# Performance work log

Hardware: AMD Instinct MI355X
Metric: run time of the kernel (lower is better)

The kernel has to match this reference:

```python
import jax, jax.numpy as jnp
import numpy as np

DEGREE = 8
D = 512
K = 256
O = 512
N = 65536


def setup_inputs() -> dict:
    key = jax.random.key(0)
    ks = jax.random.split(key, 4)
    z = jax.random.normal(ks[0], (N, D), dtype=jnp.float32)
    T0 = jnp.ones((K,), dtype=jnp.float32)
    # T[i-1] corresponds to parameter T_i, i = 1..DEGREE, each [K, D]
    T = jax.random.normal(ks[1], (DEGREE, K, D), dtype=jnp.float32) * 0.02
    C_w = jax.random.normal(ks[2], (O, K), dtype=jnp.float32) * (1.0 / np.sqrt(K))
    C_b = jnp.zeros((O,), dtype=jnp.float32)
    return {"z": z, "T0": T0, "T": T, "C_w": C_w, "C_b": C_b}


def reference(z, T0, T, C_w, C_b):
    # z: [N, D]; T: [DEGREE, K, D]; recurrence over polynomial degree n:
    #   out_n = (z @ ((2n-1)/n * T_n).T) * out_{n-1} - (n-1)/n * out_{n-2}
    z = z.reshape(-1, D)
    out_prev2 = T0                                  # degree 0, [K] (broadcasts over N)
    out_prev1 = jnp.einsum('nd,kd->nk', z, T[0])    # degree 1, [N, K]
    for n in range(2, DEGREE + 1):
        a = (2.0 * n - 1.0) / n
        b = (n - 1.0) / n
        cur = jnp.einsum('nd,kd->nk', z, a * T[n - 1]) * out_prev1 - b * out_prev2
        out_prev2, out_prev1 = out_prev1, cur
    # layer_C applied to out_list[degree]
    return out_prev1 @ C_w.T + C_b
```

## Files before the change

kernel.cpp:

```cpp
#include <hip/hip_runtime.h>
#include <hip/hip_fp16.h>
#include <cstdint>

#define NROWS 65536
#define DIM   512
#define KDIM  256
#define ODIM  512
#define DEG   8
#define ZN    (NROWS * DIM)
#define TN    (DEG * KDIM * DIM)
#define CWN   (ODIM * KDIM)

typedef _Float16 f16x8 __attribute__((ext_vector_type(8)));
typedef float    f32x4 __attribute__((ext_vector_type(4)));


__device__ __forceinline__ void gld_lds16(const void* g, void* l) {
  __builtin_amdgcn_global_load_lds(
      (const __attribute__((address_space(1))) unsigned int*)g,
      (__attribute__((address_space(3))) unsigned int*)l, 16, 0, 0);
}

__device__ __forceinline__ unsigned pack2h(float a, float b) {
  union { _Float16 h[2]; unsigned u; } x;
  x.h[0] = (_Float16)a; x.h[1] = (_Float16)b;
  return x.u;
}

__device__ __forceinline__ int swz(int row, int chunk) {
  return (row << 7) | (((chunk + row) & 7) << 4);
}


__global__ void k_convert(const float* __restrict__ z,
                          const float* __restrict__ T,
                          const float* __restrict__ Cw,
                          _Float16* __restrict__ z16,
                          _Float16* __restrict__ Tb,
                          _Float16* __restrict__ Cwb) {
  long e = ((long)blockIdx.x * 256 + threadIdx.x) * 4;
  const float* src;
  _Float16* dst;
  float s = 1.0f;
  if (e < ZN) {
    src = z + e; dst = z16 + e;
  } else {
    long o = e - ZN;
    if (o < TN) {
      int n = (int)(o >> 17);
      s = (n == 0) ? 1.0f : (float)(2 * n + 1) / (float)(n + 1);
      src = T + o; dst = Tb + o;
    } else {
      long c = o - TN;
      if (c >= CWN) return;
      src = Cw + c; dst = Cwb + c;
    }
  }
  float4 v = *(const float4*)src;
  uint2 p; p.x = pack2h(v.x * s, v.y * s); p.y = pack2h(v.z * s, v.w * s);
  *(uint2*)dst = p;
}


__launch_bounds__(256, 3)
__global__ void k_poly(const _Float16* __restrict__ z16,
                       const float* __restrict__ T0,
                       const _Float16* __restrict__ Tb,
                       _Float16* __restrict__ u8) {
  __shared__ __align__(16) uint16_t As[128 * 64];
  __shared__ __align__(16) uint16_t Bs[128 * 64];

  const int tid = threadIdx.x;
  const int wave = tid >> 6, lane = tid & 63;

  const int id = blockIdx.x;
  const int super = id >> 8, rem = id & 255;
  const int kg = rem >> 4;
  const int rt = (super << 4) | (rem & 15);
  const int r0 = rt << 7;
  const int k0 = kg << 4;

  const int m_l = lane & 15, kq = lane >> 4;
  const int wrow = wave << 5;

  f32x4 acc[DEG][2];
#pragma unroll
  for (int n = 0; n < DEG; n++)
#pragma unroll
    for (int a = 0; a < 2; a++)
      acc[n][a] = (f32x4){0.f, 0.f, 0.f, 0.f};

  const _Float16* aptr[4];
  const _Float16* bptr[4];
  int lofs[4];
#pragma unroll
  for (int j = 0; j < 4; j++) {
    int lin = (j << 8) + tid;
    int row = lin >> 3;
    int c = ((lin & 7) - row) & 7;
    lofs[j] = lin << 4;
    aptr[j] = z16 + (size_t)(r0 + row) * DIM + (c << 3);
    int n = row >> 4, kk = row & 15;
    bptr[j] = Tb + (size_t)((n << 8) + k0 + kk) * DIM + (c << 3);
  }

  for (int it = 0; it < DIM / 64; it++) {
    __syncthreads();
#pragma unroll
    for (int j = 0; j < 4; j++) gld_lds16(aptr[j], (char*)As + lofs[j]);
#pragma unroll
    for (int j = 0; j < 4; j++) gld_lds16(bptr[j], (char*)Bs + lofs[j]);
#pragma unroll
    for (int j = 0; j < 4; j++) { aptr[j] += 64; bptr[j] += 64; }
    __syncthreads();

#pragma unroll
    for (int ks = 0; ks < 2; ks++) {
      const int chunk = (ks << 2) + kq;
      f16x8 af[2];
#pragma unroll
      for (int mf = 0; mf < 2; mf++)
        af[mf] = *(const f16x8*)((char*)As + swz(wrow + (mf << 4) + m_l, chunk));
#pragma unroll
      for (int n = 0; n < DEG; n++) {
        f16x8 bv = *(const f16x8*)((char*)Bs + swz((n << 4) + m_l, chunk));
#pragma unroll
        for (int mf = 0; mf < 2; mf++)
          acc[n][mf] = __builtin_amdgcn_mfma_f32_16x16x32_f16(
              af[mf], bv, acc[n][mf], 0, 0, 0);
      }
    }
  }

  const float bcoef[7] = {1.f/2.f, 2.f/3.f, 3.f/4.f, 4.f/5.f,
                          5.f/6.f, 6.f/7.f, 7.f/8.f};
  const int col = k0 + m_l;
  const float t0v = T0[col];
#pragma unroll
  for (int mf = 0; mf < 2; mf++) {
    f32x4 up2 = {t0v, t0v, t0v, t0v};
    f32x4 up1 = acc[0][mf];
#pragma unroll
    for (int n = 2; n <= DEG; n++) {
      f32x4 cur = acc[n - 1][mf] * up1 - bcoef[n - 2] * up2;
      up2 = up1; up1 = cur;
    }
    const int rbase = r0 + wrow + (mf << 4) + (kq << 2);
#pragma unroll
    for (int r = 0; r < 4; r++)
      u8[(size_t)(rbase + r) * KDIM + col] = (_Float16)up1[r];
  }
}


__launch_bounds__(256, 4)
__global__ void k_out(const _Float16* __restrict__ u8,
                      const _Float16* __restrict__ Cwb,
                      const float* __restrict__ Cb,
                      float* __restrict__ out) {
  __shared__ __align__(16) uint16_t As[128 * 64];
  __shared__ __align__(16) uint16_t Bs[64 * 64];

  const int tid = threadIdx.x;
  const int wave = tid >> 6, lane = tid & 63;

  const int id = blockIdx.x;
  const int super = id >> 7, rem = id & 127;
  const int cg = rem >> 4;
  const int rt = (super << 4) | (rem & 15);
  const int r0 = rt << 7;
  const int c0 = cg << 6;

  const int m_l = lane & 15, kq = lane >> 4;
  const int wrow = wave << 5;

  f32x4 acc[2][4];
#pragma unroll
  for (int a = 0; a < 2; a++)
#pragma unroll
    for (int b = 0; b < 4; b++)
      acc[a][b] = (f32x4){0.f, 0.f, 0.f, 0.f};

  const _Float16* aptr[4];
  const _Float16* bptr[2];
  int lofsA[4], lofsB[2];
#pragma unroll
  for (int j = 0; j < 4; j++) {
    int lin = (j << 8) + tid;
    int row = lin >> 3;
    int c = ((lin & 7) - row) & 7;
    lofsA[j] = lin << 4;
    aptr[j] = u8 + (size_t)(r0 + row) * KDIM + (c << 3);
  }
#pragma unroll
  for (int j = 0; j < 2; j++) {
    int lin = (j << 8) + tid;
    int row = lin >> 3;
    int c = ((lin & 7) - row) & 7;
    lofsB[j] = lin << 4;
    bptr[j] = Cwb + (size_t)(c0 + row) * KDIM + (c << 3);
  }

  for (int it = 0; it < KDIM / 64; it++) {
    __syncthreads();
#pragma unroll
    for (int j = 0; j < 4; j++) gld_lds16(aptr[j], (char*)As + lofsA[j]);
#pragma unroll
    for (int j = 0; j < 2; j++) gld_lds16(bptr[j], (char*)Bs + lofsB[j]);
#pragma unroll
    for (int j = 0; j < 4; j++) aptr[j] += 64;
#pragma unroll
    for (int j = 0; j < 2; j++) bptr[j] += 64;
    __syncthreads();

#pragma unroll
    for (int ks = 0; ks < 2; ks++) {
      const int chunk = (ks << 2) + kq;
      f16x8 af[2];
#pragma unroll
      for (int mf = 0; mf < 2; mf++)
        af[mf] = *(const f16x8*)((char*)As + swz(wrow + (mf << 4) + m_l, chunk));
#pragma unroll
      for (int kf = 0; kf < 4; kf++) {
        f16x8 bv = *(const f16x8*)((char*)Bs + swz((kf << 4) + m_l, chunk));
#pragma unroll
        for (int mf = 0; mf < 2; mf++)
          acc[mf][kf] = __builtin_amdgcn_mfma_f32_16x16x32_f16(
              af[mf], bv, acc[mf][kf], 0, 0, 0);
      }
    }
  }

#pragma unroll
  for (int kf = 0; kf < 4; kf++) {
    const int col = c0 + (kf << 4) + m_l;
    const float cb = Cb[col];
#pragma unroll
    for (int mf = 0; mf < 2; mf++) {
      const int rbase = r0 + wrow + (mf << 4) + (kq << 2);
#pragma unroll
      for (int r = 0; r < 4; r++)
        out[(size_t)(rbase + r) * ODIM + col] = acc[mf][kf][r] + cb;
    }
  }
}


extern "C" void kernel_launch(void* const* d_in, const int* in_sizes, int n_in,
                              void* d_out, int out_size, void* d_ws, size_t ws_size,
                              hipStream_t stream) {
  const float* z  = (const float*)d_in[0];
  const float* T0 = (const float*)d_in[1];
  const float* T  = (const float*)d_in[2];
  const float* Cw = (const float*)d_in[3];
  const float* Cb = (const float*)d_in[4];
  float* out = (float*)d_out;

  char* ws = (char*)d_ws;
  _Float16* z16 = (_Float16*)ws;
  _Float16* Tb  = (_Float16*)(ws + (size_t)ZN * 2);
  _Float16* Cwb = (_Float16*)(ws + (size_t)ZN * 2 + (size_t)TN * 2);
  _Float16* u8  = (_Float16*)(ws + (size_t)ZN * 2 + (size_t)TN * 2 + (size_t)CWN * 2);

  k_convert<<<33920, 256, 0, stream>>>(z, T, Cw, z16, Tb, Cwb);
  k_poly<<<8192, 256, 0, stream>>>(z16, T0, Tb, u8);
  k_out<<<4096, 256, 0, stream>>>(u8, Cwb, Cb, out);
}
```

Before: 389.2 us.

## Double row tile to 256 in poly and output GEMMs, widen convert to 8 elements

Both GEMM kernels now use a 256-row tile per block, with each wave covering 64 rows, so every loaded B tile (T slices or C_w) is reused across twice as many MFMAs. The grouped block-index swizzle is dropped in favour of a plain row-major block order. The convert kernel now handles 8 elements per thread with 16-byte stores. The trade-off is more registers and LDS per block, so occupancy hints drop to 2 and 3 blocks per CU, which leaves less latency hiding with the single-buffered loads.

```diff
diff --git a/kernel.cpp b/kernel.cpp
--- a/kernel.cpp
+++ b/kernel.cpp
@@ -38,7 +38,7 @@
                           _Float16* __restrict__ z16,
                           _Float16* __restrict__ Tb,
                           _Float16* __restrict__ Cwb) {
-  long e = ((long)blockIdx.x * 256 + threadIdx.x) * 4;
+  long e = ((long)blockIdx.x * 256 + threadIdx.x) * 8;
   const float* src;
   _Float16* dst;
   float s = 1.0f;
@@ -56,76 +56,86 @@
       src = Cw + c; dst = Cwb + c;
     }
   }
-  float4 v = *(const float4*)src;
-  uint2 p; p.x = pack2h(v.x * s, v.y * s); p.y = pack2h(v.z * s, v.w * s);
-  *(uint2*)dst = p;
-}
-
-
-__launch_bounds__(256, 3)
+  float4 v0 = *(const float4*)src;
+  float4 v1 = *(const float4*)(src + 4);
+  uint4 p;
+  p.x = pack2h(v0.x * s, v0.y * s); p.y = pack2h(v0.z * s, v0.w * s);
+  p.z = pack2h(v1.x * s, v1.y * s); p.w = pack2h(v1.z * s, v1.w * s);
+  *(uint4*)dst = p;
+}
+
+
+__launch_bounds__(256, 2)
 __global__ void k_poly(const _Float16* __restrict__ z16,
                        const float* __restrict__ T0,
                        const _Float16* __restrict__ Tb,
                        _Float16* __restrict__ u8) {
-  __shared__ __align__(16) uint16_t As[128 * 64];
+  __shared__ __align__(16) uint16_t As[256 * 64];
   __shared__ __align__(16) uint16_t Bs[128 * 64];
 
   const int tid = threadIdx.x;
   const int wave = tid >> 6, lane = tid & 63;
 
   const int id = blockIdx.x;
-  const int super = id >> 8, rem = id & 255;
-  const int kg = rem >> 4;
-  const int rt = (super << 4) | (rem & 15);
-  const int r0 = rt << 7;
+  const int rt = id >> 4, kg = id & 15;
+  const int r0 = rt << 8;
   const int k0 = kg << 4;
 
   const int m_l = lane & 15, kq = lane >> 4;
-  const int wrow = wave << 5;
-
-  f32x4 acc[DEG][2];
+  const int wrow = wave << 6;
+
+  f32x4 acc[DEG][4];
 #pragma unroll
   for (int n = 0; n < DEG; n++)
 #pragma unroll
-    for (int a = 0; a < 2; a++)
+    for (int a = 0; a < 4; a++)
       acc[n][a] = (f32x4){0.f, 0.f, 0.f, 0.f};
 
-  const _Float16* aptr[4];
+  const _Float16* aptr[8];
   const _Float16* bptr[4];
-  int lofs[4];
+  int lofsA[8], lofsB[4];
+#pragma unroll
+  for (int j = 0; j < 8; j++) {
+    int lin = (j << 8) + tid;
+    int row = lin >> 3;
+    int c = ((lin & 7) - row) & 7;
+    lofsA[j] = lin << 4;
+    aptr[j] = z16 + (size_t)(r0 + row) * DIM + (c << 3);
+  }
 #pragma unroll
   for (int j = 0; j < 4; j++) {
     int lin = (j << 8) + tid;
     int row = lin >> 3;
     int c = ((lin & 7) - row) & 7;
-    lofs[j] = lin << 4;
-    aptr[j] = z16 + (size_t)(r0 + row) * DIM + (c << 3);
     int n = row >> 4, kk = row & 15;
+    lofsB[j] = lin << 4;
     bptr[j] = Tb + (size_t)((n << 8) + k0 + kk) * DIM + (c << 3);
   }
 
   for (int it = 0; it < DIM / 64; it++) {
     __syncthreads();
 #pragma unroll
-    for (int j = 0; j < 4; j++) gld_lds16(aptr[j], (char*)As + lofs[j]);
-#pragma unroll
-    for (int j = 0; j < 4; j++) gld_lds16(bptr[j], (char*)Bs + lofs[j]);
-#pragma unroll
-    for (int j = 0; j < 4; j++) { aptr[j] += 64; bptr[j] += 64; }
+    for (int j = 0; j < 8; j++) gld_lds16(aptr[j], (char*)As + lofsA[j]);
+#pragma unroll
+    for (int j = 0; j < 4; j++) gld_lds16(bptr[j], (char*)Bs + lofsB[j]);
+#pragma unroll
+    for (int j = 0; j < 8; j++) aptr[j] += 64;
+#pragma unroll
+    for (int j = 0; j < 4; j++) bptr[j] += 64;
     __syncthreads();
 
 #pragma unroll
     for (int ks = 0; ks < 2; ks++) {
       const int chunk = (ks << 2) + kq;
-      f16x8 af[2];
-#pragma unroll
-      for (int mf = 0; mf < 2; mf++)
+      f16x8 af[4];
+#pragma unroll
+      for (int mf = 0; mf < 4; mf++)
         af[mf] = *(const f16x8*)((char*)As + swz(wrow + (mf << 4) + m_l, chunk));
 #pragma unroll
       for (int n = 0; n < DEG; n++) {
         f16x8 bv = *(const f16x8*)((char*)Bs + swz((n << 4) + m_l, chunk));
 #pragma unroll
-        for (int mf = 0; mf < 2; mf++)
+        for (int mf = 0; mf < 4; mf++)
           acc[n][mf] = __builtin_amdgcn_mfma_f32_16x16x32_f16(
               af[mf], bv, acc[n][mf], 0, 0, 0);
       }
@@ -137,7 +147,7 @@
   const int col = k0 + m_l;
   const float t0v = T0[col];
 #pragma unroll
-  for (int mf = 0; mf < 2; mf++) {
+  for (int mf = 0; mf < 4; mf++) {
     f32x4 up2 = {t0v, t0v, t0v, t0v};
     f32x4 up1 = acc[0][mf];
 #pragma unroll
@@ -153,39 +163,37 @@
 }
 
 
-__launch_bounds__(256, 4)
+__launch_bounds__(256, 3)
 __global__ void k_out(const _Float16* __restrict__ u8,
                       const _Float16* __restrict__ Cwb,
                       const float* __restrict__ Cb,
                       float* __restrict__ out) {
-  __shared__ __align__(16) uint16_t As[128 * 64];
+  __shared__ __align__(16) uint16_t As[256 * 64];
   __shared__ __align__(16) uint16_t Bs[64 * 64];
 
   const int tid = threadIdx.x;
   const int wave = tid >> 6, lane = tid & 63;
 
   const int id = blockIdx.x;
-  const int super = id >> 7, rem = id & 127;
-  const int cg = rem >> 4;
-  const int rt = (super << 4) | (rem & 15);
-  const int r0 = rt << 7;
+  const int rt = id >> 3, cg = id & 7;
+  const int r0 = rt << 8;
   const int c0 = cg << 6;
 
   const int m_l = lane & 15, kq = lane >> 4;
-  const int wrow = wave << 5;
-
-  f32x4 acc[2][4];
-#pragma unroll
-  for (int a = 0; a < 2; a++)
+  const int wrow = wave << 6;
+
+  f32x4 acc[4][4];
+#pragma unroll
+  for (int a = 0; a < 4; a++)
 #pragma unroll
     for (int b = 0; b < 4; b++)
       acc[a][b] = (f32x4){0.f, 0.f, 0.f, 0.f};
 
-  const _Float16* aptr[4];
+  const _Float16* aptr[8];
   const _Float16* bptr[2];
-  int lofsA[4], lofsB[2];
-#pragma unroll
-  for (int j = 0; j < 4; j++) {
+  int lofsA[8], lofsB[2];
+#pragma unroll
+  for (int j = 0; j < 8; j++) {
     int lin = (j << 8) + tid;
     int row = lin >> 3;
     int c = ((lin & 7) - row) & 7;
@@ -204,11 +212,11 @@
   for (int it = 0; it < KDIM / 64; it++) {
     __syncthreads();
 #pragma unroll
-    for (int j = 0; j < 4; j++) gld_lds16(aptr[j], (char*)As + lofsA[j]);
+    for (int j = 0; j < 8; j++) gld_lds16(aptr[j], (char*)As + lofsA[j]);
 #pragma unroll
     for (int j = 0; j < 2; j++) gld_lds16(bptr[j], (char*)Bs + lofsB[j]);
 #pragma unroll
-    for (int j = 0; j < 4; j++) aptr[j] += 64;
+    for (int j = 0; j < 8; j++) aptr[j] += 64;
 #pragma unroll
     for (int j = 0; j < 2; j++) bptr[j] += 64;
     __syncthreads();
@@ -216,15 +224,15 @@
 #pragma unroll
     for (int ks = 0; ks < 2; ks++) {
       const int chunk = (ks << 2) + kq;
-      f16x8 af[2];
-#pragma unroll
-      for (int mf = 0; mf < 2; mf++)
+      f16x8 af[4];
+#pragma unroll
+      for (int mf = 0; mf < 4; mf++)
         af[mf] = *(const f16x8*)((char*)As + swz(wrow + (mf << 4) + m_l, chunk));
 #pragma unroll
       for (int kf = 0; kf < 4; kf++) {
         f16x8 bv = *(const f16x8*)((char*)Bs + swz((kf << 4) + m_l, chunk));
 #pragma unroll
-        for (int mf = 0; mf < 2; mf++)
+        for (int mf = 0; mf < 4; mf++)
           acc[mf][kf] = __builtin_amdgcn_mfma_f32_16x16x32_f16(
               af[mf], bv, acc[mf][kf], 0, 0, 0);
       }
@@ -236,7 +244,7 @@
     const int col = c0 + (kf << 4) + m_l;
     const float cb = Cb[col];
 #pragma unroll
-    for (int mf = 0; mf < 2; mf++) {
+    for (int mf = 0; mf < 4; mf++) {
       const int rbase = r0 + wrow + (mf << 4) + (kq << 2);
 #pragma unroll
       for (int r = 0; r < 4; r++)
@@ -262,7 +270,7 @@
   _Float16* Cwb = (_Float16*)(ws + (size_t)ZN * 2 + (size_t)TN * 2);
   _Float16* u8  = (_Float16*)(ws + (size_t)ZN * 2 + (size_t)TN * 2 + (size_t)CWN * 2);
 
-  k_convert<<<33920, 256, 0, stream>>>(z, T, Cw, z16, Tb, Cwb);
-  k_poly<<<8192, 256, 0, stream>>>(z16, T0, Tb, u8);
-  k_out<<<4096, 256, 0, stream>>>(u8, Cwb, Cb, out);
-}
+  k_convert<<<16960, 256, 0, stream>>>(z, T, Cw, z16, Tb, Cwb);
+  k_poly<<<4096, 256, 0, stream>>>(z16, T0, Tb, u8);
+  k_out<<<2048, 256, 0, stream>>>(u8, Cwb, Cb, out);
+}
```

Measured after the change: 405.8 us. 1.04x slower.
